# Optimization experiments

Hardware: AMD Instinct MI355X
Metric: run time of the kernel (lower is better)

Reference implementation:

```python
import jax, jax.numpy as jnp
import numpy as np

N = 20000
E = 640000
IN_DIM = 128
HID = 128
OUT = 64


def setup_inputs() -> dict:
    key = jax.random.key(0)
    ks = jax.random.split(key, 16)
    s = 0.05
    inp = {
        'feat': jax.random.normal(ks[0], (N, IN_DIM), jnp.float32),
        'edge_index': jax.random.randint(ks[1], (2, E), 0, N, jnp.int64),
        # GCNConv params
        'W_gcn': jax.random.normal(ks[2], (IN_DIM, HID), jnp.float32) * s,
        'b_gcn': jnp.zeros((HID,), jnp.float32),
        # SAGEConv params (lin_l: aggregated neighbors w/ bias; lin_r: root, no bias)
        'W_sage_l': jax.random.normal(ks[3], (HID, HID), jnp.float32) * s,
        'b_sage_l': jnp.zeros((HID,), jnp.float32),
        'W_sage_r': jax.random.normal(ks[4], (HID, HID), jnp.float32) * s,
        # policy MLP
        'W1': jax.random.normal(ks[5], (HID, HID), jnp.float32) * s,
        'b1': jnp.zeros((HID,), jnp.float32),
        'W2': jax.random.normal(ks[6], (HID, HID), jnp.float32) * s,
        'b2': jnp.zeros((HID,), jnp.float32),
        'W3': jax.random.normal(ks[7], (HID, OUT), jnp.float32) * s,
        'b3': jnp.zeros((OUT,), jnp.float32),
        # value head
        'Wv': jax.random.normal(ks[8], (HID, 1), jnp.float32) * s,
        'bv': jnp.zeros((1,), jnp.float32),
    }
    return inp


def _gcn(feat, src, dst, W, b):
    # PyG GCNConv: add self loops, sym-normalize by deg^-1/2 on both ends
    loop = jnp.arange(N, dtype=src.dtype)
    s = jnp.concatenate([src, loop])
    d = jnp.concatenate([dst, loop])
    deg = jax.ops.segment_sum(jnp.ones_like(d, jnp.float32), d, num_segments=N)
    dinv = jnp.where(deg > 0, jax.lax.rsqrt(deg), 0.0)
    x = feat @ W  # [N, HID]
    msg = x[s] * (dinv[s] * dinv[d])[:, None]  # [E+N, HID]
    return jax.ops.segment_sum(msg, d, num_segments=N) + b


def _sage_mean(h, src, dst, Wl, bl, Wr):
    # PyG SAGEConv(aggr='mean'): lin_l(mean_neigh) + lin_r(root)
    neigh_sum = jax.ops.segment_sum(h[src], dst, num_segments=N)
    cnt = jax.ops.segment_sum(jnp.ones_like(dst, jnp.float32), dst, num_segments=N)
    mean = neigh_sum / jnp.maximum(cnt, 1.0)[:, None]
    return mean @ Wl + bl + h @ Wr


def reference(feat, edge_index, W_gcn, b_gcn, W_sage_l, b_sage_l, W_sage_r,
              W1, b1, W2, b2, W3, b3, Wv, bv):
    src, dst = edge_index[0], edge_index[1]
    h = jax.nn.relu(_gcn(feat, src, dst, W_gcn, b_gcn))
    h = jax.nn.relu(_sage_mean(h, src, dst, W_sage_l, b_sage_l, W_sage_r))
    # policy MLP (GELU exact, matching torch nn.GELU default)
    z = jax.nn.gelu(h @ W1 + b1, approximate=False)
    z = jax.nn.gelu(z @ W2 + b2, approximate=False)
    means = z @ W3 + b3  # [N, OUT]
    values = (h @ Wv + bv)[:, 0]  # [N]
    return (means, values)
```

## Files before the change

kernel.cpp:

```cpp
#include <hip/hip_runtime.h>
#include <math.h>


#define CAP 96

typedef __attribute__((ext_vector_type(8))) short short8;
typedef __attribute__((ext_vector_type(4))) float floatx4;

__device__ __forceinline__ unsigned short f2b(float f) {
    unsigned u = __float_as_uint(f);
    unsigned r = (u + 0x7fffu + ((u >> 16) & 1u)) >> 16;
    return (unsigned short)r;
}
__device__ __forceinline__ float b2f(unsigned short h) {
    return __uint_as_float(((unsigned)h) << 16);
}
__device__ __forceinline__ float b2f_lo(unsigned v) {
    return __uint_as_float(v << 16);
}
__device__ __forceinline__ float b2f_hi(unsigned v) {
    return __uint_as_float(v & 0xffff0000u);
}
__device__ __forceinline__ floatx4 MFMA(short8 a, short8 b, floatx4 c) {
    return __builtin_amdgcn_mfma_f32_16x16x32_bf16(a, b, c, 0, 0, 0);
}
__device__ __forceinline__ float gelu_exact(float x) {
    return 0.5f * x * (1.0f + erff(x * 0.70710678118654752440f));
}

#define FRAG(P, ct, ks, lane) (*(const short8*)((P) + (((((ct)*4 + (ks))*64) + (lane)) << 3)))


__global__ __launch_bounds__(256) void pack_zero_kernel(
    int* __restrict__ cnt, int N,
    const float* Wg, const float* Wsl, const float* Wsr,
    const float* W1, const float* W2, const float* W3,
    unsigned short* Pg, unsigned short* Psl, unsigned short* Psr,
    unsigned short* P1, unsigned short* P2, unsigned short* P3)
{
    int t = blockIdx.x * 256 + threadIdx.x;
    for (int i = t; i < N; i += 11264) cnt[i] = 0;
    const float* W; unsigned short* P; int NC = 128; int base;
    if (t < 2048)       { W = Wg;  P = Pg;  base = t; }
    else if (t < 4096)  { W = Wsl; P = Psl; base = t - 2048; }
    else if (t < 6144)  { W = Wsr; P = Psr; base = t - 4096; }
    else if (t < 8192)  { W = W1;  P = P1;  base = t - 6144; }
    else if (t < 10240) { W = W2;  P = P2;  base = t - 8192; }
    else if (t < 11264) { W = W3;  P = P3;  base = t - 10240; NC = 64; }
    else return;
    int l  = base & 63;
    int ks = (base >> 6) & 3;
    int ct = base >> 8;
    int n  = ct * 16 + (l & 15);
    int k0 = ks * 32 + ((l >> 4) << 3);
    short8 v;
    #pragma unroll
    for (int j = 0; j < 8; j++) v[j] = (short)f2b(W[(size_t)(k0 + j) * NC + n]);
    *(short8*)(P + ((size_t)base << 3)) = v;
}


__global__ __launch_bounds__(256) void fill_gemm_kernel(
    const int* __restrict__ eidx, int E,
    int* __restrict__ cnt, int* __restrict__ col,
    const float* __restrict__ feat,
    const unsigned short* __restrict__ Pg,
    unsigned short* __restrict__ xs, int M, int fillBlocks, int PS)
{
    if ((int)blockIdx.x < fillBlocks) {
        int chunk = blockIdx.x >> 3;
        int p = blockIdx.x & 7;
        int lo = p * PS;
        int hi = lo + PS;
        int e0 = chunk * 2048;
        int e1 = e0 + 2048 < E ? e0 + 2048 : E;
        for (int e = e0 + (int)threadIdx.x; e < e1; e += 256) {
            int d = eidx[E + e];
            if (d >= lo && d < hi) {
                int r = atomicAdd(&cnt[d], 1);
                if (r < CAP) col[d * CAP + r] = eidx[e];
            }
        }
        return;
    }
    int bid = blockIdx.x - fillBlocks;
    int w = bid * 4 + (threadIdx.x >> 6);
    if (w >= (M / 16) * 2) return;
    int lane = threadIdx.x & 63;
    int m = lane & 15, quad = lane >> 4;
    int rt = w >> 1, ch = w & 1;
    const float* arow = feat + (size_t)(rt * 16 + m) * 128;
    short8 a[4];
    #pragma unroll
    for (int ks = 0; ks < 4; ks++) {
        float4 f0 = *(const float4*)(arow + ks * 32 + quad * 8);
        float4 f1 = *(const float4*)(arow + ks * 32 + quad * 8 + 4);
        short8 s;
        s[0] = (short)f2b(f0.x); s[1] = (short)f2b(f0.y);
        s[2] = (short)f2b(f0.z); s[3] = (short)f2b(f0.w);
        s[4] = (short)f2b(f1.x); s[5] = (short)f2b(f1.y);
        s[6] = (short)f2b(f1.z); s[7] = (short)f2b(f1.w);
        a[ks] = s;
    }
    #pragma unroll
    for (int ct = 0; ct < 4; ct++) {
        floatx4 acc = {0.f, 0.f, 0.f, 0.f};
        #pragma unroll
        for (int ks = 0; ks < 4; ks++)
            acc = MFMA(a[ks], FRAG(Pg, ch * 4 + ct, ks, lane), acc);
        #pragma unroll
        for (int reg = 0; reg < 4; reg++)
            xs[(size_t)(rt * 16 + quad * 4 + reg) * 128 + (ch * 4 + ct) * 16 + m] =
                f2b(acc[reg]);
    }
}


template<bool GCN>
__global__ __launch_bounds__(256) void agg_kernel(
    const unsigned short* __restrict__ X, const int* __restrict__ cnt,
    const int* __restrict__ col, const float* __restrict__ bias,
    unsigned short* __restrict__ Y, int N)
{
    int w = (int)((blockIdx.x * 256 + threadIdx.x) >> 6);
    if (w >= N) return;
    int lane = threadIdx.x & 63;
    int g = lane >> 4, t = lane & 15;
    const uint4* Xq = (const uint4*)X;

    int deg = cnt[w];
    int n = deg < CAP ? deg : CAP;
    int beg = w * CAP, end = beg + n;

    float acc[8] = {0.f, 0.f, 0.f, 0.f, 0.f, 0.f, 0.f, 0.f};

    int e = beg + g;
    for (; e + 4 < end; e += 8) {
        int s0 = col[e];
        int s1 = col[e + 4];
        float sc0 = 1.0f, sc1 = 1.0f;
        if (GCN) {
            sc0 = rsqrtf((float)(cnt[s0] + 1));
            sc1 = rsqrtf((float)(cnt[s1] + 1));
        }
        uint4 q0 = Xq[(size_t)s0 * 16 + t];
        uint4 q1 = Xq[(size_t)s1 * 16 + t];
        acc[0] = fmaf(b2f_lo(q0.x), sc0, acc[0]);
        acc[1] = fmaf(b2f_hi(q0.x), sc0, acc[1]);
        acc[2] = fmaf(b2f_lo(q0.y), sc0, acc[2]);
        acc[3] = fmaf(b2f_hi(q0.y), sc0, acc[3]);
        acc[4] = fmaf(b2f_lo(q0.z), sc0, acc[4]);
        acc[5] = fmaf(b2f_hi(q0.z), sc0, acc[5]);
        acc[6] = fmaf(b2f_lo(q0.w), sc0, acc[6]);
        acc[7] = fmaf(b2f_hi(q0.w), sc0, acc[7]);
        acc[0] = fmaf(b2f_lo(q1.x), sc1, acc[0]);
        acc[1] = fmaf(b2f_hi(q1.x), sc1, acc[1]);
        acc[2] = fmaf(b2f_lo(q1.y), sc1, acc[2]);
        acc[3] = fmaf(b2f_hi(q1.y), sc1, acc[3]);
        acc[4] = fmaf(b2f_lo(q1.z), sc1, acc[4]);
        acc[5] = fmaf(b2f_hi(q1.z), sc1, acc[5]);
        acc[6] = fmaf(b2f_lo(q1.w), sc1, acc[6]);
        acc[7] = fmaf(b2f_hi(q1.w), sc1, acc[7]);
    }
    if (e < end) {
        int s0 = col[e];
        float sc0 = GCN ? rsqrtf((float)(cnt[s0] + 1)) : 1.0f;
        uint4 q0 = Xq[(size_t)s0 * 16 + t];
        acc[0] = fmaf(b2f_lo(q0.x), sc0, acc[0]);
        acc[1] = fmaf(b2f_hi(q0.x), sc0, acc[1]);
        acc[2] = fmaf(b2f_lo(q0.y), sc0, acc[2]);
        acc[3] = fmaf(b2f_hi(q0.y), sc0, acc[3]);
        acc[4] = fmaf(b2f_lo(q0.z), sc0, acc[4]);
        acc[5] = fmaf(b2f_hi(q0.z), sc0, acc[5]);
        acc[6] = fmaf(b2f_lo(q0.w), sc0, acc[6]);
        acc[7] = fmaf(b2f_hi(q0.w), sc0, acc[7]);
    }

    #pragma unroll
    for (int i = 0; i < 8; i++) {
        acc[i] += __shfl_xor(acc[i], 16);
        acc[i] += __shfl_xor(acc[i], 32);
    }
    if (g == 0) {
        float out[8];
        if (GCN) {
            float dw = rsqrtf((float)(deg + 1));
            uint4 q = Xq[(size_t)w * 16 + t];
            acc[0] = fmaf(b2f_lo(q.x), dw, acc[0]);
            acc[1] = fmaf(b2f_hi(q.x), dw, acc[1]);
            acc[2] = fmaf(b2f_lo(q.y), dw, acc[2]);
            acc[3] = fmaf(b2f_hi(q.y), dw, acc[3]);
            acc[4] = fmaf(b2f_lo(q.z), dw, acc[4]);
            acc[5] = fmaf(b2f_hi(q.z), dw, acc[5]);
            acc[6] = fmaf(b2f_lo(q.w), dw, acc[6]);
            acc[7] = fmaf(b2f_hi(q.w), dw, acc[7]);
            float4 b0 = *(const float4*)(bias + t * 8);
            float4 b1 = *(const float4*)(bias + t * 8 + 4);
            out[0] = fmaxf(fmaf(acc[0], dw, b0.x), 0.f);
            out[1] = fmaxf(fmaf(acc[1], dw, b0.y), 0.f);
            out[2] = fmaxf(fmaf(acc[2], dw, b0.z), 0.f);
            out[3] = fmaxf(fmaf(acc[3], dw, b0.w), 0.f);
            out[4] = fmaxf(fmaf(acc[4], dw, b1.x), 0.f);
            out[5] = fmaxf(fmaf(acc[5], dw, b1.y), 0.f);
            out[6] = fmaxf(fmaf(acc[6], dw, b1.z), 0.f);
            out[7] = fmaxf(fmaf(acc[7], dw, b1.w), 0.f);
        } else {
            float rc = 1.0f / (float)(deg > 0 ? deg : 1);
            #pragma unroll
            for (int i = 0; i < 8; i++) out[i] = acc[i] * rc;
        }
        uint4 r;
        r.x = (unsigned)f2b(out[0]) | ((unsigned)f2b(out[1]) << 16);
        r.y = (unsigned)f2b(out[2]) | ((unsigned)f2b(out[3]) << 16);
        r.z = (unsigned)f2b(out[4]) | ((unsigned)f2b(out[5]) << 16);
        r.w = (unsigned)f2b(out[6]) | ((unsigned)f2b(out[7]) << 16);
        ((uint4*)Y)[(size_t)w * 16 + t] = r;
    }
}


__global__ __launch_bounds__(256) void sage_mlp_kernel(
    const unsigned short* __restrict__ mean, const unsigned short* __restrict__ h1,
    const unsigned short* __restrict__ Psl, const unsigned short* __restrict__ Psr,
    const float* __restrict__ bsl,
    const unsigned short* __restrict__ P1, const float* __restrict__ b1,
    const unsigned short* __restrict__ P2, const float* __restrict__ b2,
    const unsigned short* __restrict__ P3, const float* __restrict__ b3,
    const float* __restrict__ Wv, const float* __restrict__ bv,
    float* __restrict__ means, float* __restrict__ values, int M)
{
    __shared__ unsigned short z[4][16 * 136];
    int widx = threadIdx.x >> 6, lane = threadIdx.x & 63;
    int w = blockIdx.x * 4 + widx;
    if (w >= M / 16) return;
    int m = lane & 15, quad = lane >> 4;
    unsigned short* zt = &z[widx][0];
    int r0 = w * 16;

    short8 am[4], ar[4];
    #pragma unroll
    for (int ks = 0; ks < 4; ks++) {
        am[ks] = *(const short8*)(mean + (size_t)(r0 + m) * 128 + ks * 32 + quad * 8);
        ar[ks] = *(const short8*)(h1   + (size_t)(r0 + m) * 128 + ks * 32 + quad * 8);
    }

    float vpart[4] = {0.f, 0.f, 0.f, 0.f};
    #pragma unroll
    for (int ct = 0; ct < 8; ct++) {
        floatx4 acc = {0.f, 0.f, 0.f, 0.f};
        #pragma unroll
        for (int ks = 0; ks < 4; ks++) acc = MFMA(am[ks], FRAG(Psl, ct, ks, lane), acc);
        #pragma unroll
        for (int ks = 0; ks < 4; ks++) acc = MFMA(ar[ks], FRAG(Psr, ct, ks, lane), acc);
        float bb = bsl[ct * 16 + m];
        float wv = Wv[ct * 16 + m];
        #pragma unroll
        for (int reg = 0; reg < 4; reg++) {
            float o = fmaxf(acc[reg] + bb, 0.f);
            vpart[reg] = fmaf(o, wv, vpart[reg]);
            zt[(quad * 4 + reg) * 136 + ct * 16 + m] = f2b(o);
        }
    }
    #pragma unroll
    for (int off = 1; off <= 8; off <<= 1) {
        #pragma unroll
        for (int reg = 0; reg < 4; reg++)
            vpart[reg] += __shfl_xor(vpart[reg], off);
    }
    if (m == 0) {
        float bvv = bv[0];
        #pragma unroll
        for (int reg = 0; reg < 4; reg++)
            values[r0 + quad * 4 + reg] = vpart[reg] + bvv;
    }

    short8 a1[4];
    #pragma unroll
    for (int ks = 0; ks < 4; ks++)
        a1[ks] = *(const short8*)(zt + m * 136 + ks * 32 + quad * 8);

    #pragma unroll
    for (int ct = 0; ct < 8; ct++) {
        floatx4 acc = {0.f, 0.f, 0.f, 0.f};
        #pragma unroll
        for (int ks = 0; ks < 4; ks++) acc = MFMA(a1[ks], FRAG(P1, ct, ks, lane), acc);
        float bb = b1[ct * 16 + m];
        #pragma unroll
        for (int reg = 0; reg < 4; reg++)
            zt[(quad * 4 + reg) * 136 + ct * 16 + m] = f2b(gelu_exact(acc[reg] + bb));
    }
    short8 a2[4];
    #pragma unroll
    for (int ks = 0; ks < 4; ks++)
        a2[ks] = *(const short8*)(zt + m * 136 + ks * 32 + quad * 8);

    #pragma unroll
    for (int ct = 0; ct < 8; ct++) {
        floatx4 acc = {0.f, 0.f, 0.f, 0.f};
        #pragma unroll
        for (int ks = 0; ks < 4; ks++) acc = MFMA(a2[ks], FRAG(P2, ct, ks, lane), acc);
        float bb = b2[ct * 16 + m];
        #pragma unroll
        for (int reg = 0; reg < 4; reg++)
            zt[(quad * 4 + reg) * 136 + ct * 16 + m] = f2b(gelu_exact(acc[reg] + bb));
    }
    short8 a3[4];
    #pragma unroll
    for (int ks = 0; ks < 4; ks++)
        a3[ks] = *(const short8*)(zt + m * 136 + ks * 32 + quad * 8);

    #pragma unroll
    for (int ct = 0; ct < 4; ct++) {
        floatx4 acc = {0.f, 0.f, 0.f, 0.f};
        #pragma unroll
        for (int ks = 0; ks < 4; ks++) acc = MFMA(a3[ks], FRAG(P3, ct, ks, lane), acc);
        float bb = b3[ct * 16 + m];
        #pragma unroll
        for (int reg = 0; reg < 4; reg++)
            means[(size_t)(r0 + quad * 4 + reg) * 64 + ct * 16 + m] = acc[reg] + bb;
    }
}


extern "C" void kernel_launch(void* const* d_in, const int* in_sizes, int n_in,
                              void* d_out, int out_size, void* d_ws, size_t ws_size,
                              hipStream_t stream) {
    const float* feat  = (const float*)d_in[0];
    const int*   eidx  = (const int*)d_in[1];
    const float* W_gcn = (const float*)d_in[2];
    const float* b_gcn = (const float*)d_in[3];
    const float* W_sl  = (const float*)d_in[4];
    const float* b_sl  = (const float*)d_in[5];
    const float* W_sr  = (const float*)d_in[6];
    const float* W1    = (const float*)d_in[7];
    const float* b1    = (const float*)d_in[8];
    const float* W2    = (const float*)d_in[9];
    const float* b2    = (const float*)d_in[10];
    const float* W3    = (const float*)d_in[11];
    const float* b3    = (const float*)d_in[12];
    const float* Wv    = (const float*)d_in[13];
    const float* bv    = (const float*)d_in[14];

    const int N = in_sizes[0] / 128;
    const int E = in_sizes[1] / 2;

    char* ws = (char*)d_ws;
    size_t off = 0;
    auto alloc = [&](size_t bytes) -> void* {
        void* p = ws + off;
        off += (bytes + 255) & ~(size_t)255;
        return p;
    };
    int*   cnt = (int*)alloc((size_t)N * 4);
    int*   col = (int*)alloc((size_t)N * CAP * 4);
    unsigned short* xs   = (unsigned short*)alloc((size_t)N * 128 * 2);
    unsigned short* h1   = (unsigned short*)alloc((size_t)N * 128 * 2);
    unsigned short* mean = (unsigned short*)alloc((size_t)N * 128 * 2);
    unsigned short* Pg   = (unsigned short*)alloc(2048 * 8 * 2);
    unsigned short* Psl  = (unsigned short*)alloc(2048 * 8 * 2);
    unsigned short* Psr  = (unsigned short*)alloc(2048 * 8 * 2);
    unsigned short* P1   = (unsigned short*)alloc(2048 * 8 * 2);
    unsigned short* P2   = (unsigned short*)alloc(2048 * 8 * 2);
    unsigned short* P3   = (unsigned short*)alloc(1024 * 8 * 2);

    pack_zero_kernel<<<44, 256, 0, stream>>>(
        cnt, N, W_gcn, W_sl, W_sr, W1, W2, W3,
        Pg, Psl, Psr, P1, P2, P3);

    const int PS = (N + 7) / 8;
    const int fillBlocks = ((E + 2047) / 2048) * 8;
    const int gemmBlocks = ((N / 16) * 2 + 3) / 4;
    fill_gemm_kernel<<<fillBlocks + gemmBlocks, 256, 0, stream>>>(
        eidx, E, cnt, col, feat, Pg, xs, N, fillBlocks, PS);

    const int agrid = (N + 3) / 4;
    agg_kernel<true><<<agrid, 256, 0, stream>>>(xs, cnt, col, b_gcn, h1, N);
    agg_kernel<false><<<agrid, 256, 0, stream>>>(h1, cnt, col, nullptr, mean, N);

    sage_mlp_kernel<<<(N / 16 + 3) / 4, 256, 0, stream>>>(
        mean, h1, Psl, Psr, b_sl, P1, b1, P2, b2, P3, b3, Wv, bv,
        (float*)d_out, (float*)d_out + (size_t)N * 64, N);
}
```

Before: 187.4 us.

## Fuse SAGE mean aggregation into the MLP kernel and split columns across warps

The second neighbor-mean aggregation moves into the SAGE/MLP kernel. Each block gathers mean features for its 16 rows into shared memory, so the separate aggregation launch and the global mean buffer round-trip go away. The four warps of a block now share one 16-row tile and each computes a slice of the output columns, which adds block-wide barriers and a shared-memory reduction for the value head. This gives fewer rows per block than before, since the four warps no longer each handle their own tile, and the gather phase stays serialized before the MFMA phases.

```diff
diff --git a/kernel.cpp b/kernel.cpp
--- a/kernel.cpp
+++ b/kernel.cpp
@@ -116,8 +116,7 @@
 }
 
 
-template<bool GCN>
-__global__ __launch_bounds__(256) void agg_kernel(
+__global__ __launch_bounds__(256) void agg_gcn_kernel(
     const unsigned short* __restrict__ X, const int* __restrict__ cnt,
     const int* __restrict__ col, const float* __restrict__ bias,
     unsigned short* __restrict__ Y, int N)
@@ -138,11 +137,8 @@
     for (; e + 4 < end; e += 8) {
         int s0 = col[e];
         int s1 = col[e + 4];
-        float sc0 = 1.0f, sc1 = 1.0f;
-        if (GCN) {
-            sc0 = rsqrtf((float)(cnt[s0] + 1));
-            sc1 = rsqrtf((float)(cnt[s1] + 1));
-        }
+        float sc0 = rsqrtf((float)(cnt[s0] + 1));
+        float sc1 = rsqrtf((float)(cnt[s1] + 1));
         uint4 q0 = Xq[(size_t)s0 * 16 + t];
         uint4 q1 = Xq[(size_t)s1 * 16 + t];
         acc[0] = fmaf(b2f_lo(q0.x), sc0, acc[0]);
@@ -164,7 +160,7 @@
     }
     if (e < end) {
         int s0 = col[e];
-        float sc0 = GCN ? rsqrtf((float)(cnt[s0] + 1)) : 1.0f;
+        float sc0 = rsqrtf((float)(cnt[s0] + 1));
         uint4 q0 = Xq[(size_t)s0 * 16 + t];
         acc[0] = fmaf(b2f_lo(q0.x), sc0, acc[0]);
         acc[1] = fmaf(b2f_hi(q0.x), sc0, acc[1]);
@@ -182,33 +178,27 @@
         acc[i] += __shfl_xor(acc[i], 32);
     }
     if (g == 0) {
+        float dw = rsqrtf((float)(deg + 1));
+        uint4 q = Xq[(size_t)w * 16 + t];
+        acc[0] = fmaf(b2f_lo(q.x), dw, acc[0]);
+        acc[1] = fmaf(b2f_hi(q.x), dw, acc[1]);
+        acc[2] = fmaf(b2f_lo(q.y), dw, acc[2]);
+        acc[3] = fmaf(b2f_hi(q.y), dw, acc[3]);
+        acc[4] = fmaf(b2f_lo(q.z), dw, acc[4]);
+        acc[5] = fmaf(b2f_hi(q.z), dw, acc[5]);
+        acc[6] = fmaf(b2f_lo(q.w), dw, acc[6]);
+        acc[7] = fmaf(b2f_hi(q.w), dw, acc[7]);
+        float4 b0 = *(const float4*)(bias + t * 8);
+        float4 b1 = *(const float4*)(bias + t * 8 + 4);
         float out[8];
-        if (GCN) {
-            float dw = rsqrtf((float)(deg + 1));
-            uint4 q = Xq[(size_t)w * 16 + t];
-            acc[0] = fmaf(b2f_lo(q.x), dw, acc[0]);
-            acc[1] = fmaf(b2f_hi(q.x), dw, acc[1]);
-            acc[2] = fmaf(b2f_lo(q.y), dw, acc[2]);
-            acc[3] = fmaf(b2f_hi(q.y), dw, acc[3]);
-            acc[4] = fmaf(b2f_lo(q.z), dw, acc[4]);
-            acc[5] = fmaf(b2f_hi(q.z), dw, acc[5]);
-            acc[6] = fmaf(b2f_lo(q.w), dw, acc[6]);
-            acc[7] = fmaf(b2f_hi(q.w), dw, acc[7]);
-            float4 b0 = *(const float4*)(bias + t * 8);
-            float4 b1 = *(const float4*)(bias + t * 8 + 4);
-            out[0] = fmaxf(fmaf(acc[0], dw, b0.x), 0.f);
-            out[1] = fmaxf(fmaf(acc[1], dw, b0.y), 0.f);
-            out[2] = fmaxf(fmaf(acc[2], dw, b0.z), 0.f);
-            out[3] = fmaxf(fmaf(acc[3], dw, b0.w), 0.f);
-            out[4] = fmaxf(fmaf(acc[4], dw, b1.x), 0.f);
-            out[5] = fmaxf(fmaf(acc[5], dw, b1.y), 0.f);
-            out[6] = fmaxf(fmaf(acc[6], dw, b1.z), 0.f);
-            out[7] = fmaxf(fmaf(acc[7], dw, b1.w), 0.f);
-        } else {
-            float rc = 1.0f / (float)(deg > 0 ? deg : 1);
-            #pragma unroll
-            for (int i = 0; i < 8; i++) out[i] = acc[i] * rc;
-        }
+        out[0] = fmaxf(fmaf(acc[0], dw, b0.x), 0.f);
+        out[1] = fmaxf(fmaf(acc[1], dw, b0.y), 0.f);
+        out[2] = fmaxf(fmaf(acc[2], dw, b0.z), 0.f);
+        out[3] = fmaxf(fmaf(acc[3], dw, b0.w), 0.f);
+        out[4] = fmaxf(fmaf(acc[4], dw, b1.x), 0.f);
+        out[5] = fmaxf(fmaf(acc[5], dw, b1.y), 0.f);
+        out[6] = fmaxf(fmaf(acc[6], dw, b1.z), 0.f);
+        out[7] = fmaxf(fmaf(acc[7], dw, b1.w), 0.f);
         uint4 r;
         r.x = (unsigned)f2b(out[0]) | ((unsigned)f2b(out[1]) << 16);
         r.y = (unsigned)f2b(out[2]) | ((unsigned)f2b(out[3]) << 16);
@@ -219,46 +209,97 @@
 }
 
 
-__global__ __launch_bounds__(256) void sage_mlp_kernel(
-    const unsigned short* __restrict__ mean, const unsigned short* __restrict__ h1,
+__global__ __launch_bounds__(256) void sage_fused_kernel(
+    const unsigned short* __restrict__ h1, const int* __restrict__ cnt,
+    const int* __restrict__ col,
     const unsigned short* __restrict__ Psl, const unsigned short* __restrict__ Psr,
     const float* __restrict__ bsl,
     const unsigned short* __restrict__ P1, const float* __restrict__ b1,
     const unsigned short* __restrict__ P2, const float* __restrict__ b2,
     const unsigned short* __restrict__ P3, const float* __restrict__ b3,
     const float* __restrict__ Wv, const float* __restrict__ bv,
-    float* __restrict__ means, float* __restrict__ values, int M)
+    float* __restrict__ means, float* __restrict__ values, int N)
 {
-    __shared__ unsigned short z[4][16 * 136];
+    __shared__ unsigned short zm[16 * 136];
+    __shared__ unsigned short za[16 * 136];
+    __shared__ float vp[16][4];
     int widx = threadIdx.x >> 6, lane = threadIdx.x & 63;
-    int w = blockIdx.x * 4 + widx;
-    if (w >= M / 16) return;
-    int m = lane & 15, quad = lane >> 4;
-    unsigned short* zt = &z[widx][0];
-    int r0 = w * 16;
+    int r0 = blockIdx.x * 16;
+    if (r0 >= N) return;
+    int g = lane >> 4, t = lane & 15;
+    const uint4* Xq = (const uint4*)h1;
+
+    for (int rr = 0; rr < 4; rr++) {
+        int w = r0 + widx * 4 + rr;
+        int deg = cnt[w];
+        int n = deg < CAP ? deg : CAP;
+        int beg = w * CAP, end = beg + n;
+        float acc[8] = {0.f, 0.f, 0.f, 0.f, 0.f, 0.f, 0.f, 0.f};
+        int e = beg + g;
+        for (; e + 4 < end; e += 8) {
+            int s0 = col[e];
+            int s1 = col[e + 4];
+            uint4 q0 = Xq[(size_t)s0 * 16 + t];
+            uint4 q1 = Xq[(size_t)s1 * 16 + t];
+            acc[0] += b2f_lo(q0.x); acc[1] += b2f_hi(q0.x);
+            acc[2] += b2f_lo(q0.y); acc[3] += b2f_hi(q0.y);
+            acc[4] += b2f_lo(q0.z); acc[5] += b2f_hi(q0.z);
+            acc[6] += b2f_lo(q0.w); acc[7] += b2f_hi(q0.w);
+            acc[0] += b2f_lo(q1.x); acc[1] += b2f_hi(q1.x);
+            acc[2] += b2f_lo(q1.y); acc[3] += b2f_hi(q1.y);
+            acc[4] += b2f_lo(q1.z); acc[5] += b2f_hi(q1.z);
+            acc[6] += b2f_lo(q1.w); acc[7] += b2f_hi(q1.w);
+        }
+        if (e < end) {
+            int s0 = col[e];
+            uint4 q0 = Xq[(size_t)s0 * 16 + t];
+            acc[0] += b2f_lo(q0.x); acc[1] += b2f_hi(q0.x);
+            acc[2] += b2f_lo(q0.y); acc[3] += b2f_hi(q0.y);
+            acc[4] += b2f_lo(q0.z); acc[5] += b2f_hi(q0.z);
+            acc[6] += b2f_lo(q0.w); acc[7] += b2f_hi(q0.w);
+        }
+        #pragma unroll
+        for (int i = 0; i < 8; i++) {
+            acc[i] += __shfl_xor(acc[i], 16);
+            acc[i] += __shfl_xor(acc[i], 32);
+        }
+        if (g == 0) {
+            float rc = 1.0f / (float)(deg > 0 ? deg : 1);
+            uint4 r;
+            r.x = (unsigned)f2b(acc[0] * rc) | ((unsigned)f2b(acc[1] * rc) << 16);
+            r.y = (unsigned)f2b(acc[2] * rc) | ((unsigned)f2b(acc[3] * rc) << 16);
+            r.z = (unsigned)f2b(acc[4] * rc) | ((unsigned)f2b(acc[5] * rc) << 16);
+            r.w = (unsigned)f2b(acc[6] * rc) | ((unsigned)f2b(acc[7] * rc) << 16);
+            *(uint4*)(zm + (widx * 4 + rr) * 136 + t * 8) = r;
+        }
+    }
+    __syncthreads();
+
+    int m = t, quad = g;
 
     short8 am[4], ar[4];
     #pragma unroll
     for (int ks = 0; ks < 4; ks++) {
-        am[ks] = *(const short8*)(mean + (size_t)(r0 + m) * 128 + ks * 32 + quad * 8);
-        ar[ks] = *(const short8*)(h1   + (size_t)(r0 + m) * 128 + ks * 32 + quad * 8);
+        am[ks] = *(const short8*)(zm + m * 136 + ks * 32 + quad * 8);
+        ar[ks] = *(const short8*)(h1 + (size_t)(r0 + m) * 128 + ks * 32 + quad * 8);
     }
 
     float vpart[4] = {0.f, 0.f, 0.f, 0.f};
     #pragma unroll
-    for (int ct = 0; ct < 8; ct++) {
+    for (int ci = 0; ci < 2; ci++) {
+        int ct = widx * 2 + ci;
         floatx4 acc = {0.f, 0.f, 0.f, 0.f};
         #pragma unroll
         for (int ks = 0; ks < 4; ks++) acc = MFMA(am[ks], FRAG(Psl, ct, ks, lane), acc);
         #pragma unroll
         for (int ks = 0; ks < 4; ks++) acc = MFMA(ar[ks], FRAG(Psr, ct, ks, lane), acc);
         float bb = bsl[ct * 16 + m];
-        float wv = Wv[ct * 16 + m];
+        float wvv = Wv[ct * 16 + m];
         #pragma unroll
         for (int reg = 0; reg < 4; reg++) {
             float o = fmaxf(acc[reg] + bb, 0.f);
-            vpart[reg] = fmaf(o, wv, vpart[reg]);
-            zt[(quad * 4 + reg) * 136 + ct * 16 + m] = f2b(o);
+            vpart[reg] = fmaf(o, wvv, vpart[reg]);
+            za[(quad * 4 + reg) * 136 + ct * 16 + m] = f2b(o);
         }
     }
     #pragma unroll
@@ -268,49 +309,58 @@
             vpart[reg] += __shfl_xor(vpart[reg], off);
     }
     if (m == 0) {
-        float bvv = bv[0];
-        #pragma unroll
-        for (int reg = 0; reg < 4; reg++)
-            values[r0 + quad * 4 + reg] = vpart[reg] + bvv;
+        #pragma unroll
+        for (int reg = 0; reg < 4; reg++)
+            vp[quad * 4 + reg][widx] = vpart[reg];
+    }
+    __syncthreads();
+
+    if (threadIdx.x < 16) {
+        float v = vp[threadIdx.x][0] + vp[threadIdx.x][1]
+                + vp[threadIdx.x][2] + vp[threadIdx.x][3];
+        values[r0 + threadIdx.x] = v + bv[0];
     }
 
     short8 a1[4];
     #pragma unroll
     for (int ks = 0; ks < 4; ks++)
-        a1[ks] = *(const short8*)(zt + m * 136 + ks * 32 + quad * 8);
-
-    #pragma unroll
-    for (int ct = 0; ct < 8; ct++) {
+        a1[ks] = *(const short8*)(za + m * 136 + ks * 32 + quad * 8);
+    #pragma unroll
+    for (int ci = 0; ci < 2; ci++) {
+        int ct = widx * 2 + ci;
         floatx4 acc = {0.f, 0.f, 0.f, 0.f};
         #pragma unroll
         for (int ks = 0; ks < 4; ks++) acc = MFMA(a1[ks], FRAG(P1, ct, ks, lane), acc);
         float bb = b1[ct * 16 + m];
         #pragma unroll
         for (int reg = 0; reg < 4; reg++)
-            zt[(quad * 4 + reg) * 136 + ct * 16 + m] = f2b(gelu_exact(acc[reg] + bb));
-    }
+            zm[(quad * 4 + reg) * 136 + ct * 16 + m] = f2b(gelu_exact(acc[reg] + bb));
+    }
+    __syncthreads();
+
     short8 a2[4];
     #pragma unroll
     for (int ks = 0; ks < 4; ks++)
-        a2[ks] = *(const short8*)(zt + m * 136 + ks * 32 + quad * 8);
-
-    #pragma unroll
-    for (int ct = 0; ct < 8; ct++) {
+        a2[ks] = *(const short8*)(zm + m * 136 + ks * 32 + quad * 8);
+    #pragma unroll
+    for (int ci = 0; ci < 2; ci++) {
+        int ct = widx * 2 + ci;
         floatx4 acc = {0.f, 0.f, 0.f, 0.f};
         #pragma unroll
         for (int ks = 0; ks < 4; ks++) acc = MFMA(a2[ks], FRAG(P2, ct, ks, lane), acc);
         float bb = b2[ct * 16 + m];
         #pragma unroll
         for (int reg = 0; reg < 4; reg++)
-            zt[(quad * 4 + reg) * 136 + ct * 16 + m] = f2b(gelu_exact(acc[reg] + bb));
-    }
+            za[(quad * 4 + reg) * 136 + ct * 16 + m] = f2b(gelu_exact(acc[reg] + bb));
+    }
+    __syncthreads();
+
     short8 a3[4];
     #pragma unroll
     for (int ks = 0; ks < 4; ks++)
-        a3[ks] = *(const short8*)(zt + m * 136 + ks * 32 + quad * 8);
-
-    #pragma unroll
-    for (int ct = 0; ct < 4; ct++) {
+        a3[ks] = *(const short8*)(za + m * 136 + ks * 32 + quad * 8);
+    {
+        int ct = widx;
         floatx4 acc = {0.f, 0.f, 0.f, 0.f};
         #pragma unroll
         for (int ks = 0; ks < 4; ks++) acc = MFMA(a3[ks], FRAG(P3, ct, ks, lane), acc);
@@ -355,7 +405,6 @@
     int*   col = (int*)alloc((size_t)N * CAP * 4);
     unsigned short* xs   = (unsigned short*)alloc((size_t)N * 128 * 2);
     unsigned short* h1   = (unsigned short*)alloc((size_t)N * 128 * 2);
-    unsigned short* mean = (unsigned short*)alloc((size_t)N * 128 * 2);
     unsigned short* Pg   = (unsigned short*)alloc(2048 * 8 * 2);
     unsigned short* Psl  = (unsigned short*)alloc(2048 * 8 * 2);
     unsigned short* Psr  = (unsigned short*)alloc(2048 * 8 * 2);
@@ -374,10 +423,9 @@
         eidx, E, cnt, col, feat, Pg, xs, N, fillBlocks, PS);
 
     const int agrid = (N + 3) / 4;
-    agg_kernel<true><<<agrid, 256, 0, stream>>>(xs, cnt, col, b_gcn, h1, N);
-    agg_kernel<false><<<agrid, 256, 0, stream>>>(h1, cnt, col, nullptr, mean, N);
-
-    sage_mlp_kernel<<<(N / 16 + 3) / 4, 256, 0, stream>>>(
-        mean, h1, Psl, Psr, b_sl, P1, b1, P2, b2, P3, b3, Wv, bv,
+    agg_gcn_kernel<<<agrid, 256, 0, stream>>>(xs, cnt, col, b_gcn, h1, N);
+
+    sage_fused_kernel<<<(N + 15) / 16, 256, 0, stream>>>(
+        h1, cnt, col, Psl, Psr, b_sl, P1, b1, P2, b2, P3, b3, Wv, bv,
         (float*)d_out, (float*)d_out + (size_t)N * 64, N);
 }
```

Result: faster. 180.7 us (-3.6%).
